# Kernel optimization log

Measured on AMD Instinct MI355X. Metric: run time of the kernel, lower is better.

Reference implementation:

```python
import jax, jax.numpy as jnp
import numpy as np

B, L1, D, H = 4, 1024, 512, 16
L, R = 8192, 8
DFF = 4 * D
DH = D // H  # head dim = 32


def _ln(x, g, b, eps=1e-5):
    mu = x.mean(-1, keepdims=True)
    var = ((x - mu) ** 2).mean(-1, keepdims=True)
    return (x - mu) * jax.lax.rsqrt(var + eps) * g + b


def _mha(q_in, k_in, v_in, Wq, bq, Wk, bk, Wv, bv, Wo, bo):
    # Informer FullAttention (mask_flag=False), scale = 1/sqrt(head_dim), mix=False
    Bq, Lq, _ = q_in.shape
    S = k_in.shape[1]
    q = (q_in @ Wq.T + bq).reshape(Bq, Lq, H, DH)
    k = (k_in @ Wk.T + bk).reshape(Bq, S, H, DH)
    v = (v_in @ Wv.T + bv).reshape(Bq, S, H, DH)
    scores = jnp.einsum('blhe,bshe->bhls', q, k) * (1.0 / jnp.sqrt(jnp.float32(DH)))
    A = jax.nn.softmax(scores, axis=-1)
    out = jnp.einsum('bhls,bshd->blhd', A, v).reshape(Bq, Lq, D)
    return out @ Wo.T + bo


def _p(key, *shape):
    return jax.random.normal(key, shape, jnp.float32) * 0.02


def setup_inputs() -> dict:
    ks = jax.random.split(jax.random.key(0), 16)
    inp = {
        'x': jax.random.normal(ks[0], (B, L1, D), jnp.float32),
        'global_feat': jax.random.normal(ks[1], (B, D, L), jnp.float32),
        'conv_w': _p(ks[2], D, D), 'conv_b': jnp.zeros((D,), jnp.float32),
        'sWq': _p(ks[3], D, D), 'sbq': jnp.zeros((D,), jnp.float32),
        'sWk': _p(ks[4], D, D), 'sbk': jnp.zeros((D,), jnp.float32),
        'sWv': _p(ks[5], D, D), 'sbv': jnp.zeros((D,), jnp.float32),
        'sWo': _p(ks[6], D, D), 'sbo': jnp.zeros((D,), jnp.float32),
        'cWq': _p(ks[7], D, D), 'cbq': jnp.zeros((D,), jnp.float32),
        'cWk': _p(ks[8], D, D), 'cbk': jnp.zeros((D,), jnp.float32),
        'cWv': _p(ks[9], D, D), 'cbv': jnp.zeros((D,), jnp.float32),
        'cWo': _p(ks[10], D, D), 'cbo': jnp.zeros((D,), jnp.float32),
        'ffn_w1': _p(ks[11], DFF, D), 'ffn_b1': jnp.zeros((DFF,), jnp.float32),
        'ffn_w2': _p(ks[12], D, DFF), 'ffn_b2': jnp.zeros((D,), jnp.float32),
        'ln1_g': jnp.ones((D,), jnp.float32), 'ln1_b': jnp.zeros((D,), jnp.float32),
        'ln2_g': jnp.ones((D,), jnp.float32), 'ln2_b': jnp.zeros((D,), jnp.float32),
        'ln3_g': jnp.ones((D,), jnp.float32), 'ln3_b': jnp.zeros((D,), jnp.float32),
    }
    return inp


def reference(x, global_feat, conv_w, conv_b,
              sWq, sbq, sWk, sbk, sWv, sbv, sWo, sbo,
              cWq, cbq, cWk, cbk, cWv, cbv, cWo, cbo,
              ffn_w1, ffn_b1, ffn_w2, ffn_b2,
              ln1_g, ln1_b, ln2_g, ln2_b, ln3_g, ln3_b):
    b, c, length = global_feat.shape
    win = 2 * R  # step == window_size -> non-overlapping windows
    nw = (length - win) // win + 1
    w = global_feat[:, :, :nw * win].reshape(b, c, nw, win)
    # norm over singleton last dim == |max - min| per (b, c, window)
    stat = jnp.abs(w.max(-1) - w.min(-1))  # [B, C, NW]
    # pointwise Conv1d(512,512,1) + relu
    res = jax.nn.relu(jnp.einsum('oc,bcn->bon', conv_w, stat) + conv_b[None, :, None])
    cross = res.transpose(0, 2, 1)  # [B, NW, D] tokens for cross attention
    # EncoderLayer3: self-attn -> cross-attn -> FFN, post-LN residuals
    h = _ln(x + _mha(x, x, x, sWq, sbq, sWk, sbk, sWv, sbv, sWo, sbo), ln1_g, ln1_b)
    h = _ln(h + _mha(h, cross, cross, cWq, cbq, cWk, cbk, cWv, cbv, cWo, cbo), ln2_g, ln2_b)
    y = jax.nn.gelu(h @ ffn_w1.T + ffn_b1) @ ffn_w2.T + ffn_b2
    out = _ln(h + y, ln3_g, ln3_b)
    return out.transpose(0, 2, 1)  # [B, D, L1]
```

## Files before the change

kernel.cpp:

```cpp
#include <hip/hip_runtime.h>
#include <stdint.h>
#include <math.h>


typedef short  s16x8 __attribute__((ext_vector_type(8)));
typedef float  f32x4 __attribute__((ext_vector_type(4)));

__device__ inline unsigned short f2bf(float f) {
  uint32_t u = __builtin_bit_cast(uint32_t, f);
  u += 0x7fffu + ((u >> 16) & 1u);
  return (unsigned short)(u >> 16);
}
__device__ inline float bf2f(unsigned short h) {
  uint32_t u = ((uint32_t)h) << 16;
  return __builtin_bit_cast(float, u);
}
__device__ inline uint32_t cvtpk_bf16(float lo, float hi) {
  uint32_t r;
  asm("v_cvt_pk_bf16_f32 %0, %1, %2" : "=v"(r) : "v"(lo), "v"(hi));
  return r;
}

#define QSCALE 0.25503486611627154f

__global__ __launch_bounds__(256) void convert_bf16_kernel(
    const float* s0, const float* s1, const float* s2, const float* s3,
    const float* s4, const float* s5, const float* s6, const float* s7,
    const float* s8, const float* s9, const float* s10, const float* s11,
    unsigned short* dst) {
  const size_t cum[13] = {0, 262144, 524288, 786432, 1048576, 1310720,
                          1572864, 1835008, 2097152, 2359296, 3407872,
                          4456448, 6553600};
  const float* srcs[12] = {s0, s1, s2, s3, s4, s5, s6, s7, s8, s9, s10, s11};
  size_t e0 = ((size_t)blockIdx.x * 256 + threadIdx.x) * 8;
  int seg = 0;
  while (e0 >= cum[seg + 1]) ++seg;
  const float* sp = srcs[seg] + (e0 - cum[seg]);
  float4 a = *(const float4*)sp;
  float4 b = *(const float4*)(sp + 4);
  unsigned short o[8] = {f2bf(a.x), f2bf(a.y), f2bf(a.z), f2bf(a.w),
                         f2bf(b.x), f2bf(b.y), f2bf(b.z), f2bf(b.w)};
  *(uint4*)&dst[e0] = *(const uint4*)o;
}

__global__ __launch_bounds__(256) void window_stat_kernel(
    const float* __restrict__ gf, unsigned short* __restrict__ statT) {
  int gidx = blockIdx.x * 256 + threadIdx.x;
  int c = gidx & 511;
  int n = (gidx >> 9) & 511;
  int b = gidx >> 18;
  const float4* p = (const float4*)(gf + ((size_t)(b * 512 + c) << 13) + n * 16);
  float4 w0 = p[0], w1 = p[1], w2 = p[2], w3 = p[3];
  float mx = w0.x, mn = w0.x;
  float vals[15] = {w0.y, w0.z, w0.w, w1.x, w1.y, w1.z, w1.w,
                    w2.x, w2.y, w2.z, w2.w, w3.x, w3.y, w3.z, w3.w};
#pragma unroll
  for (int i = 0; i < 15; ++i) {
    mx = fmaxf(mx, vals[i]);
    mn = fminf(mn, vals[i]);
  }
  statT[((size_t)(b * 512 + n) << 9) + c] = f2bf(mx - mn);
}

__global__ __launch_bounds__(256) void biascat_kernel(
    const float* __restrict__ sbq, const float* __restrict__ sbk,
    const float* __restrict__ sbv, const float* __restrict__ cbk,
    const float* __restrict__ cbv, float* __restrict__ dst) {
  int i = blockIdx.x * 256 + threadIdx.x;
  float v;
  if (i < 512) v = sbq[i];
  else if (i < 1024) v = sbk[i - 512];
  else if (i < 1536) v = sbv[i - 1024];
  else if (i < 2048) v = cbk[i - 1536];
  else v = cbv[i - 2048];
  dst[i] = v;
}

template <int ACT, int OUTBF, int SCALEQ>
__global__ __launch_bounds__(256) void gemm_bf16(
    const unsigned short* __restrict__ A, const unsigned short* __restrict__ W,
    const float* __restrict__ bias, void* __restrict__ Cout,
    int M, int N, int K) {
  __shared__ __align__(16) unsigned short As[2][64 * 32];
  __shared__ __align__(16) unsigned short Bs[2][128 * 32];
  const int t = threadIdx.x;
  const int w = t >> 6, lane = t & 63;
  const int r = lane & 15, g = lane >> 4;
  const int wm = w >> 1, wn = w & 1;
  const int m0 = blockIdx.y * 64, n0 = blockIdx.x * 128;

  auto STAGE = [&](int buf, int k0) {
    {
      int row = t >> 2, seg = t & 3;
      const unsigned short* ga = A + (size_t)(m0 + row) * K + k0 + seg * 8;
      __builtin_amdgcn_global_load_lds(
          (const __attribute__((address_space(1))) uint32_t*)ga,
          (__attribute__((address_space(3))) uint32_t*)&As[buf][t * 8], 16, 0, 0);
    }
#pragma unroll
    for (int ii = 0; ii < 2; ++ii) {
      int c = t + 256 * ii;
      int row = c >> 2, seg = c & 3;
      const unsigned short* gb = W + (size_t)(n0 + row) * K + k0 + seg * 8;
      __builtin_amdgcn_global_load_lds(
          (const __attribute__((address_space(1))) uint32_t*)gb,
          (__attribute__((address_space(3))) uint32_t*)&Bs[buf][c * 8], 16, 0, 0);
    }
  };

  f32x4 acc[2][4];
#pragma unroll
  for (int mi = 0; mi < 2; ++mi)
#pragma unroll
    for (int ni = 0; ni < 4; ++ni) acc[mi][ni] = (f32x4){0.f, 0.f, 0.f, 0.f};

  STAGE(0, 0);
  __syncthreads();
  int cur = 0;
  for (int k0 = 0; k0 < K; k0 += 32) {
    if (k0 + 32 < K) STAGE(cur ^ 1, k0 + 32);
    s16x8 af[2], bf[4];
#pragma unroll
    for (int mi = 0; mi < 2; ++mi)
      af[mi] = *(const s16x8*)&As[cur][(wm * 32 + mi * 16 + r) * 32 + g * 8];
#pragma unroll
    for (int ni = 0; ni < 4; ++ni)
      bf[ni] = *(const s16x8*)&Bs[cur][(wn * 64 + ni * 16 + r) * 32 + g * 8];
#pragma unroll
    for (int mi = 0; mi < 2; ++mi)
#pragma unroll
      for (int ni = 0; ni < 4; ++ni)
        acc[mi][ni] = __builtin_amdgcn_mfma_f32_16x16x32_bf16(
            af[mi], bf[ni], acc[mi][ni], 0, 0, 0);
    __syncthreads();
    cur ^= 1;
  }

#pragma unroll
  for (int ni = 0; ni < 4; ++ni) {
    const int col = n0 + wn * 64 + ni * 16 + r;
    const float bv = bias[col];
#pragma unroll
    for (int mi = 0; mi < 2; ++mi) {
#pragma unroll
      for (int rg = 0; rg < 4; ++rg) {
        const int row = m0 + wm * 32 + mi * 16 + g * 4 + rg;
        float v = acc[mi][ni][rg] + bv;
        if (ACT == 1) v = fmaxf(v, 0.f);
        if (ACT == 2) {
          float u = 0.7978845608028654f * (v + 0.044715f * v * v * v);
          float e = __expf(2.f * u);
          float th = 1.f - 2.f / (e + 1.f);
          v = 0.5f * v * (1.f + th);
        }
        if (SCALEQ && col < 512) v *= QSCALE;
        if (OUTBF)
          ((unsigned short*)Cout)[(size_t)row * N + col] = f2bf(v);
        else
          ((float*)Cout)[(size_t)row * N + col] = v;
      }
    }
  }
}

template <int S>
__global__ __launch_bounds__(256) void vtrans_kernel(
    const unsigned short* __restrict__ V, int vstride,
    unsigned short* __restrict__ VT) {
  const int b = blockIdx.z, h = blockIdx.y, s0 = blockIdx.x * 64;
  const int t = threadIdx.x;
  __shared__ unsigned short tile[64 * 40];
  {
    int i = t >> 2, seg = t & 3;
    *(uint4*)&tile[i * 40 + seg * 8] =
        *(const uint4*)&V[((size_t)(b * S + s0 + i)) * vstride + h * 32 + seg * 8];
  }
  __syncthreads();
  {
    int d = t >> 3, j = t & 7;
    unsigned short vals[8];
#pragma unroll
    for (int u = 0; u < 8; ++u) vals[u] = tile[(j * 8 + u) * 40 + d];
    *(uint4*)&VT[((size_t)((b * 16 + h) * 32 + d)) * S + s0 + j * 8] =
        *(const uint4*)vals;
  }
}

template <int S>
__global__ __launch_bounds__(512) void attn_mfma(
    const unsigned short* __restrict__ Q, int qstride,
    const unsigned short* __restrict__ K, int kstride,
    const unsigned short* __restrict__ VT, unsigned short* __restrict__ O) {
  constexpr int NT = S / 128;
  __shared__ __align__(16) unsigned short Kl[128 * 40];
  __shared__ __align__(16) unsigned short Vl[32 * 136];
  __shared__ __align__(16) unsigned short Pl[8][16 * 136];
  const int t = threadIdx.x;
  const int w = t >> 6, lane = t & 63;
  const int r = lane & 15, g = lane >> 4;
  const int qt = blockIdx.x, h = blockIdx.y, b = blockIdx.z;
  const int q0 = qt * 128 + w * 16;

  s16x8 qa = *(const s16x8*)&Q[((size_t)(b * 1024 + q0 + r)) * qstride + h * 32 + g * 8];

  f32x4 o0 = (f32x4){0.f, 0.f, 0.f, 0.f};
  f32x4 o1 = (f32x4){0.f, 0.f, 0.f, 0.f};
  float m = -1e30f, l = 0.f;

  for (int nt = 0; nt < NT; ++nt) {
    const int kv0 = nt * 128;
    {
      int row = t >> 2, seg = t & 3;
      *(uint4*)&Kl[row * 40 + seg * 8] =
          *(const uint4*)&K[((size_t)(b * S + kv0 + row)) * kstride + h * 32 + seg * 8];
    }
    {
      int d = t >> 4, sc = t & 15;
      *(uint4*)&Vl[d * 136 + sc * 8] =
          *(const uint4*)&VT[((size_t)((b * 16 + h) * 32 + d)) * S + kv0 + sc * 8];
    }
    __syncthreads();

    f32x4 s[8];
#pragma unroll
    for (int nb = 0; nb < 8; ++nb) {
      s16x8 ka = *(const s16x8*)&Kl[(nb * 16 + r) * 40 + g * 8];
      s[nb] = __builtin_amdgcn_mfma_f32_16x16x32_bf16(
          ka, qa, (f32x4){0.f, 0.f, 0.f, 0.f}, 0, 0, 0);
    }

    float tm = -1e30f;
#pragma unroll
    for (int nb = 0; nb < 8; ++nb) {
      float a01 = fmaxf(s[nb][0], s[nb][1]);
      float a23 = fmaxf(s[nb][2], s[nb][3]);
      tm = fmaxf(tm, fmaxf(a01, a23));
    }
    tm = fmaxf(tm, __shfl_xor(tm, 16));
    tm = fmaxf(tm, __shfl_xor(tm, 32));
    const float mnew = fmaxf(m, tm);
    const float corr = __builtin_amdgcn_exp2f(m - mnew);
    float ps = 0.f;
#pragma unroll
    for (int nb = 0; nb < 8; ++nb) {
      float p0 = __builtin_amdgcn_exp2f(s[nb][0] - mnew);
      float p1 = __builtin_amdgcn_exp2f(s[nb][1] - mnew);
      float p2 = __builtin_amdgcn_exp2f(s[nb][2] - mnew);
      float p3 = __builtin_amdgcn_exp2f(s[nb][3] - mnew);
      ps += (p0 + p1) + (p2 + p3);
      uint2 pv;
      pv.x = cvtpk_bf16(p0, p1);
      pv.y = cvtpk_bf16(p2, p3);
      *(uint2*)&Pl[w][r * 136 + nb * 16 + g * 4] = pv;
    }
    ps += __shfl_xor(ps, 16);
    ps += __shfl_xor(ps, 32);
    l = l * corr + ps;
    m = mnew;
#pragma unroll
    for (int rg = 0; rg < 4; ++rg) { o0[rg] *= corr; o1[rg] *= corr; }

#pragma unroll
    for (int ks = 0; ks < 4; ++ks) {
      s16x8 va0 = *(const s16x8*)&Vl[r * 136 + ks * 32 + g * 8];
      s16x8 va1 = *(const s16x8*)&Vl[(16 + r) * 136 + ks * 32 + g * 8];
      s16x8 pb  = *(const s16x8*)&Pl[w][r * 136 + ks * 32 + g * 8];
      o0 = __builtin_amdgcn_mfma_f32_16x16x32_bf16(va0, pb, o0, 0, 0, 0);
      o1 = __builtin_amdgcn_mfma_f32_16x16x32_bf16(va1, pb, o1, 0, 0, 0);
    }
    __syncthreads();
  }

  const float inv = 1.f / l;
  const size_t row = (size_t)(b * 1024 + q0 + r);
  uint2 w0, w1;
  w0.x = cvtpk_bf16(o0[0] * inv, o0[1] * inv);
  w0.y = cvtpk_bf16(o0[2] * inv, o0[3] * inv);
  w1.x = cvtpk_bf16(o1[0] * inv, o1[1] * inv);
  w1.y = cvtpk_bf16(o1[2] * inv, o1[3] * inv);
  *(uint2*)&O[row * 512 + h * 32 + g * 4]      = w0;
  *(uint2*)&O[row * 512 + h * 32 + 16 + g * 4] = w1;
}

template <int XBF, int ABF, int MODE>
__global__ __launch_bounds__(256) void ln_kernel(
    const void* __restrict__ X, const void* __restrict__ A,
    const float* __restrict__ gw, const float* __restrict__ bw,
    void* __restrict__ O) {
  const int rr = blockIdx.x;
  const int t = threadIdx.x;
  const size_t base = (size_t)rr * 512;
  float x0, x1, a0, a1;
  if (XBF) {
    x0 = bf2f(((const unsigned short*)X)[base + t]);
    x1 = bf2f(((const unsigned short*)X)[base + t + 256]);
  } else {
    x0 = ((const float*)X)[base + t];
    x1 = ((const float*)X)[base + t + 256];
  }
  if (ABF) {
    a0 = bf2f(((const unsigned short*)A)[base + t]);
    a1 = bf2f(((const unsigned short*)A)[base + t + 256]);
  } else {
    a0 = ((const float*)A)[base + t];
    a1 = ((const float*)A)[base + t + 256];
  }
  float v0 = x0 + a0;
  float v1 = x1 + a1;
  __shared__ float wsum[4];
  float s = v0 + v1;
#pragma unroll
  for (int of = 32; of; of >>= 1) s += __shfl_down(s, of);
  if ((t & 63) == 0) wsum[t >> 6] = s;
  __syncthreads();
  const float mean = (wsum[0] + wsum[1] + wsum[2] + wsum[3]) * (1.f / 512.f);
  __syncthreads();
  float d0 = v0 - mean, d1 = v1 - mean;
  float s2 = d0 * d0 + d1 * d1;
#pragma unroll
  for (int of = 32; of; of >>= 1) s2 += __shfl_down(s2, of);
  if ((t & 63) == 0) wsum[t >> 6] = s2;
  __syncthreads();
  const float var = (wsum[0] + wsum[1] + wsum[2] + wsum[3]) * (1.f / 512.f);
  const float rstd = rsqrtf(var + 1e-5f);
  float o0 = d0 * rstd * gw[t] + bw[t];
  float o1 = d1 * rstd * gw[t + 256] + bw[t + 256];
  if (MODE == 0) {
    ((unsigned short*)O)[base + t] = f2bf(o0);
    ((unsigned short*)O)[base + t + 256] = f2bf(o1);
  } else {
    int b = rr >> 10, l = rr & 1023;
    ((float*)O)[((size_t)(b * 512) + t) * 1024 + l] = o0;
    ((float*)O)[((size_t)(b * 512) + t + 256) * 1024 + l] = o1;
  }
}

extern "C" void kernel_launch(void* const* d_in, const int* in_sizes, int n_in,
                              void* d_out, int out_size, void* d_ws, size_t ws_size,
                              hipStream_t stream) {
  const float* x      = (const float*)d_in[0];
  const float* gf     = (const float*)d_in[1];
  const float* conv_w = (const float*)d_in[2];
  const float* conv_b = (const float*)d_in[3];
  const float* sWq = (const float*)d_in[4],  *sbq = (const float*)d_in[5];
  const float* sWk = (const float*)d_in[6],  *sbk = (const float*)d_in[7];
  const float* sWv = (const float*)d_in[8],  *sbv = (const float*)d_in[9];
  const float* sWo = (const float*)d_in[10], *sbo = (const float*)d_in[11];
  const float* cWq = (const float*)d_in[12], *cbq = (const float*)d_in[13];
  const float* cWk = (const float*)d_in[14], *cbk = (const float*)d_in[15];
  const float* cWv = (const float*)d_in[16], *cbv = (const float*)d_in[17];
  const float* cWo = (const float*)d_in[18], *cbo = (const float*)d_in[19];
  const float* fw1 = (const float*)d_in[20], *fb1 = (const float*)d_in[21];
  const float* fw2 = (const float*)d_in[22], *fb2 = (const float*)d_in[23];
  const float* ln1_g = (const float*)d_in[24], *ln1_b = (const float*)d_in[25];
  const float* ln2_g = (const float*)d_in[26], *ln2_b = (const float*)d_in[27];
  const float* ln3_g = (const float*)d_in[28], *ln3_b = (const float*)d_in[29];
  float* out = (float*)d_out;

  unsigned short* bfp = (unsigned short*)d_ws;
  unsigned short* conv_wb = bfp + 0;
  unsigned short* sWqb = bfp + 262144;
  unsigned short* cWqb = bfp + 1310720;
  unsigned short* cWkb = bfp + 1572864;
  unsigned short* cWob = bfp + 2097152;
  unsigned short* sWob = bfp + 1048576;
  unsigned short* fw1b = bfp + 2359296, *fw2b = bfp + 3407872;
  unsigned short* xbf  = bfp + 4456448;

  unsigned short* SC   = bfp + 6553600;
  unsigned short* qkvb = SC;
  unsigned short* ckvb = SC + 6291456;
  unsigned short* qcb  = SC + 8388608;
  unsigned short* vtb  = SC + 10485760;
  unsigned short* ctxb = SC + 12582912;
  unsigned short* projb= SC + 14680064;
  unsigned short* hbf  = SC + 16777216;
  unsigned short* h2bf = SC + 18874368;
  unsigned short* statTb = qcb;
  unsigned short* crossb = ctxb;
  unsigned short* midb   = qkvb;
  float* biasf = (float*)projb;

  convert_bf16_kernel<<<3200, 256, 0, stream>>>(
      conv_w, sWq, sWk, sWv, sWo, cWq, cWk, cWv, cWo, fw1, fw2, x, bfp);
  window_stat_kernel<<<4096, 256, 0, stream>>>(gf, statTb);
  biascat_kernel<<<10, 256, 0, stream>>>(sbq, sbk, sbv, cbk, cbv, biasf);

  gemm_bf16<1, 1, 0><<<dim3(4, 32), 256, 0, stream>>>(
      statTb, conv_wb, conv_b, crossb, 2048, 512, 512);
  gemm_bf16<0, 1, 1><<<dim3(12, 64), 256, 0, stream>>>(
      xbf, sWqb, biasf, qkvb, 4096, 1536, 512);
  gemm_bf16<0, 1, 0><<<dim3(8, 32), 256, 0, stream>>>(
      crossb, cWkb, biasf + 1536, ckvb, 2048, 1024, 512);

  vtrans_kernel<1024><<<dim3(16, 16, 4), 256, 0, stream>>>(qkvb + 1024, 1536, vtb);
  attn_mfma<1024><<<dim3(8, 16, 4), 512, 0, stream>>>(
      qkvb, 1536, qkvb + 512, 1536, vtb, ctxb);
  gemm_bf16<0, 1, 0><<<dim3(4, 64), 256, 0, stream>>>(
      ctxb, sWob, sbo, projb, 4096, 512, 512);
  ln_kernel<0, 1, 0><<<4096, 256, 0, stream>>>(x, projb, ln1_g, ln1_b, hbf);

  gemm_bf16<0, 1, 1><<<dim3(4, 64), 256, 0, stream>>>(
      hbf, cWqb, cbq, qcb, 4096, 512, 512);
  vtrans_kernel<512><<<dim3(8, 16, 4), 256, 0, stream>>>(ckvb + 512, 1024, vtb);
  attn_mfma<512><<<dim3(8, 16, 4), 512, 0, stream>>>(
      qcb, 512, ckvb, 1024, vtb, ctxb);
  gemm_bf16<0, 1, 0><<<dim3(4, 64), 256, 0, stream>>>(
      ctxb, cWob, cbo, projb, 4096, 512, 512);
  ln_kernel<1, 1, 0><<<4096, 256, 0, stream>>>(hbf, projb, ln2_g, ln2_b, h2bf);

  gemm_bf16<2, 1, 0><<<dim3(16, 64), 256, 0, stream>>>(
      h2bf, fw1b, fb1, midb, 4096, 2048, 512);
  gemm_bf16<0, 1, 0><<<dim3(4, 64), 256, 0, stream>>>(
      midb, fw2b, fb2, projb, 4096, 512, 2048);
  ln_kernel<1, 1, 1><<<4096, 256, 0, stream>>>(h2bf, projb, ln3_g, ln3_b, out);
}
```

Measured before the change: 380.3 us.

## Merge prep kernels, widen GEMM K-tile with swizzle, fuse V transpose, tile output transpose

Folds the bf16 conversion, window-stat and bias-concat launches into one prep kernel. The GEMM K-step grows from 32 to 64, with an XOR-swizzled LDS layout to avoid bank conflicts. Attention now reads V directly, transposes it into LDS and prefetches the next K/V tile into registers, which drops the separate vtrans launches. The final LayerNorm writes bf16 and a tiled transpose kernel produces the fp32 output, replacing the strided scattered stores. In exchange, LDS use per GEMM block doubles and the output is rounded to bf16 before the transpose, which costs some precision.

```diff
diff --git a/kernel.cpp b/kernel.cpp
--- a/kernel.cpp
+++ b/kernel.cpp
@@ -23,57 +23,58 @@
 
 #define QSCALE 0.25503486611627154f
 
-__global__ __launch_bounds__(256) void convert_bf16_kernel(
+__global__ __launch_bounds__(256) void prep_kernel(
     const float* s0, const float* s1, const float* s2, const float* s3,
     const float* s4, const float* s5, const float* s6, const float* s7,
     const float* s8, const float* s9, const float* s10, const float* s11,
-    unsigned short* dst) {
-  const size_t cum[13] = {0, 262144, 524288, 786432, 1048576, 1310720,
-                          1572864, 1835008, 2097152, 2359296, 3407872,
-                          4456448, 6553600};
-  const float* srcs[12] = {s0, s1, s2, s3, s4, s5, s6, s7, s8, s9, s10, s11};
-  size_t e0 = ((size_t)blockIdx.x * 256 + threadIdx.x) * 8;
-  int seg = 0;
-  while (e0 >= cum[seg + 1]) ++seg;
-  const float* sp = srcs[seg] + (e0 - cum[seg]);
-  float4 a = *(const float4*)sp;
-  float4 b = *(const float4*)(sp + 4);
-  unsigned short o[8] = {f2bf(a.x), f2bf(a.y), f2bf(a.z), f2bf(a.w),
-                         f2bf(b.x), f2bf(b.y), f2bf(b.z), f2bf(b.w)};
-  *(uint4*)&dst[e0] = *(const uint4*)o;
-}
-
-__global__ __launch_bounds__(256) void window_stat_kernel(
-    const float* __restrict__ gf, unsigned short* __restrict__ statT) {
-  int gidx = blockIdx.x * 256 + threadIdx.x;
-  int c = gidx & 511;
-  int n = (gidx >> 9) & 511;
-  int b = gidx >> 18;
-  const float4* p = (const float4*)(gf + ((size_t)(b * 512 + c) << 13) + n * 16);
-  float4 w0 = p[0], w1 = p[1], w2 = p[2], w3 = p[3];
-  float mx = w0.x, mn = w0.x;
-  float vals[15] = {w0.y, w0.z, w0.w, w1.x, w1.y, w1.z, w1.w,
-                    w2.x, w2.y, w2.z, w2.w, w3.x, w3.y, w3.z, w3.w};
-#pragma unroll
-  for (int i = 0; i < 15; ++i) {
-    mx = fmaxf(mx, vals[i]);
-    mn = fminf(mn, vals[i]);
-  }
-  statT[((size_t)(b * 512 + n) << 9) + c] = f2bf(mx - mn);
-}
-
-__global__ __launch_bounds__(256) void biascat_kernel(
+    unsigned short* dst,
+    const float* __restrict__ gf, unsigned short* __restrict__ statT,
     const float* __restrict__ sbq, const float* __restrict__ sbk,
     const float* __restrict__ sbv, const float* __restrict__ cbk,
-    const float* __restrict__ cbv, float* __restrict__ dst) {
-  int i = blockIdx.x * 256 + threadIdx.x;
-  float v;
-  if (i < 512) v = sbq[i];
-  else if (i < 1024) v = sbk[i - 512];
-  else if (i < 1536) v = sbv[i - 1024];
-  else if (i < 2048) v = cbk[i - 1536];
-  else v = cbv[i - 2048];
-  dst[i] = v;
+    const float* __restrict__ cbv, float* __restrict__ biasf) {
+  const int bid = blockIdx.x;
+  const int t = threadIdx.x;
+  if (bid < 3200) {
+    const size_t cum[13] = {0, 262144, 524288, 786432, 1048576, 1310720,
+                            1572864, 1835008, 2097152, 2359296, 3407872,
+                            4456448, 6553600};
+    const float* srcs[12] = {s0, s1, s2, s3, s4, s5, s6, s7, s8, s9, s10, s11};
+    size_t e0 = ((size_t)bid * 256 + t) * 8;
+    int seg = 0;
+    while (e0 >= cum[seg + 1]) ++seg;
+    const float* sp = srcs[seg] + (e0 - cum[seg]);
+    float4 a = *(const float4*)sp;
+    float4 b = *(const float4*)(sp + 4);
+    unsigned short o[8] = {f2bf(a.x), f2bf(a.y), f2bf(a.z), f2bf(a.w),
+                           f2bf(b.x), f2bf(b.y), f2bf(b.z), f2bf(b.w)};
+    *(uint4*)&dst[e0] = *(const uint4*)o;
+  } else if (bid < 7296) {
+    int gidx = (bid - 3200) * 256 + t;
+    int c = gidx & 511;
+    int n = (gidx >> 9) & 511;
+    int b = gidx >> 18;
+    const float4* p = (const float4*)(gf + ((size_t)(b * 512 + c) << 13) + n * 16);
+    float4 w0 = p[0], w1 = p[1], w2 = p[2], w3 = p[3];
+    float mx = w0.x, mn = w0.x;
+    float vals[15] = {w0.y, w0.z, w0.w, w1.x, w1.y, w1.z, w1.w,
+                      w2.x, w2.y, w2.z, w2.w, w3.x, w3.y, w3.z, w3.w};
+#pragma unroll
+    for (int i = 0; i < 15; ++i) {
+      mx = fmaxf(mx, vals[i]);
+      mn = fminf(mn, vals[i]);
+    }
+    statT[((size_t)(b * 512 + n) << 9) + c] = f2bf(mx - mn);
+  } else {
+    for (int i = t; i < 2560; i += 256) {
+      float v;
+      if (i < 512) v = sbq[i];
+      else if (i < 1024) v = sbk[i - 512];
+      else if (i < 1536) v = sbv[i - 1024];
+      else if (i < 2048) v = cbk[i - 1536];
+      else v = cbv[i - 2048];
+      biasf[i] = v;
+    }
+  }
 }
 
 template <int ACT, int OUTBF, int SCALEQ>
@@ -81,8 +82,8 @@
     const unsigned short* __restrict__ A, const unsigned short* __restrict__ W,
     const float* __restrict__ bias, void* __restrict__ Cout,
     int M, int N, int K) {
-  __shared__ __align__(16) unsigned short As[2][64 * 32];
-  __shared__ __align__(16) unsigned short Bs[2][128 * 32];
+  __shared__ __align__(16) unsigned short As[2][64 * 64];
+  __shared__ __align__(16) unsigned short Bs[2][128 * 64];
   const int t = threadIdx.x;
   const int w = t >> 6, lane = t & 63;
   const int r = lane & 15, g = lane >> 4;
@@ -90,18 +91,22 @@
   const int m0 = blockIdx.y * 64, n0 = blockIdx.x * 128;
 
   auto STAGE = [&](int buf, int k0) {
-    {
-      int row = t >> 2, seg = t & 3;
-      const unsigned short* ga = A + (size_t)(m0 + row) * K + k0 + seg * 8;
+#pragma unroll
+    for (int ii = 0; ii < 2; ++ii) {
+      int c = t + 256 * ii;
+      int row = c >> 3, sc = c & 7;
+      const unsigned short* ga =
+          A + (size_t)(m0 + row) * K + k0 + ((sc ^ (row & 7)) << 3);
       __builtin_amdgcn_global_load_lds(
           (const __attribute__((address_space(1))) uint32_t*)ga,
-          (__attribute__((address_space(3))) uint32_t*)&As[buf][t * 8], 16, 0, 0);
-    }
-#pragma unroll
-    for (int ii = 0; ii < 2; ++ii) {
+          (__attribute__((address_space(3))) uint32_t*)&As[buf][c * 8], 16, 0, 0);
+    }
+#pragma unroll
+    for (int ii = 0; ii < 4; ++ii) {
       int c = t + 256 * ii;
-      int row = c >> 2, seg = c & 3;
-      const unsigned short* gb = W + (size_t)(n0 + row) * K + k0 + seg * 8;
+      int row = c >> 3, sc = c & 7;
+      const unsigned short* gb =
+          W + (size_t)(n0 + row) * K + k0 + ((sc ^ (row & 7)) << 3);
       __builtin_amdgcn_global_load_lds(
           (const __attribute__((address_space(1))) uint32_t*)gb,
           (__attribute__((address_space(3))) uint32_t*)&Bs[buf][c * 8], 16, 0, 0);
@@ -117,21 +122,26 @@
   STAGE(0, 0);
   __syncthreads();
   int cur = 0;
-  for (int k0 = 0; k0 < K; k0 += 32) {
-    if (k0 + 32 < K) STAGE(cur ^ 1, k0 + 32);
-    s16x8 af[2], bf[4];
-#pragma unroll
-    for (int mi = 0; mi < 2; ++mi)
-      af[mi] = *(const s16x8*)&As[cur][(wm * 32 + mi * 16 + r) * 32 + g * 8];
-#pragma unroll
-    for (int ni = 0; ni < 4; ++ni)
-      bf[ni] = *(const s16x8*)&Bs[cur][(wn * 64 + ni * 16 + r) * 32 + g * 8];
-#pragma unroll
-    for (int mi = 0; mi < 2; ++mi)
+  for (int k0 = 0; k0 < K; k0 += 64) {
+    if (k0 + 64 < K) STAGE(cur ^ 1, k0 + 64);
+#pragma unroll
+    for (int ks = 0; ks < 2; ++ks) {
+      s16x8 af[2], bf[4];
+#pragma unroll
+      for (int mi = 0; mi < 2; ++mi)
+        af[mi] = *(const s16x8*)&As[cur][(wm * 32 + mi * 16 + r) * 64 +
+                                         (((ks * 4 + g) ^ (r & 7)) << 3)];
 #pragma unroll
       for (int ni = 0; ni < 4; ++ni)
-        acc[mi][ni] = __builtin_amdgcn_mfma_f32_16x16x32_bf16(
-            af[mi], bf[ni], acc[mi][ni], 0, 0, 0);
+        bf[ni] = *(const s16x8*)&Bs[cur][(wn * 64 + ni * 16 + r) * 64 +
+                                         (((ks * 4 + g) ^ (r & 7)) << 3)];
+#pragma unroll
+      for (int mi = 0; mi < 2; ++mi)
+#pragma unroll
+        for (int ni = 0; ni < 4; ++ni)
+          acc[mi][ni] = __builtin_amdgcn_mfma_f32_16x16x32_bf16(
+              af[mi], bf[ni], acc[mi][ni], 0, 0, 0);
+    }
     __syncthreads();
     cur ^= 1;
   }
@@ -164,33 +174,11 @@
 }
 
 template <int S>
-__global__ __launch_bounds__(256) void vtrans_kernel(
-    const unsigned short* __restrict__ V, int vstride,
-    unsigned short* __restrict__ VT) {
-  const int b = blockIdx.z, h = blockIdx.y, s0 = blockIdx.x * 64;
-  const int t = threadIdx.x;
-  __shared__ unsigned short tile[64 * 40];
-  {
-    int i = t >> 2, seg = t & 3;
-    *(uint4*)&tile[i * 40 + seg * 8] =
-        *(const uint4*)&V[((size_t)(b * S + s0 + i)) * vstride + h * 32 + seg * 8];
-  }
-  __syncthreads();
-  {
-    int d = t >> 3, j = t & 7;
-    unsigned short vals[8];
-#pragma unroll
-    for (int u = 0; u < 8; ++u) vals[u] = tile[(j * 8 + u) * 40 + d];
-    *(uint4*)&VT[((size_t)((b * 16 + h) * 32 + d)) * S + s0 + j * 8] =
-        *(const uint4*)vals;
-  }
-}
-
-template <int S>
 __global__ __launch_bounds__(512) void attn_mfma(
     const unsigned short* __restrict__ Q, int qstride,
     const unsigned short* __restrict__ K, int kstride,
-    const unsigned short* __restrict__ VT, unsigned short* __restrict__ O) {
+    const unsigned short* __restrict__ V, int vstride,
+    unsigned short* __restrict__ O) {
   constexpr int NT = S / 128;
   __shared__ __align__(16) unsigned short Kl[128 * 40];
   __shared__ __align__(16) unsigned short Vl[32 * 136];
@@ -200,6 +188,7 @@
   const int r = lane & 15, g = lane >> 4;
   const int qt = blockIdx.x, h = blockIdx.y, b = blockIdx.z;
   const int q0 = qt * 128 + w * 16;
+  const int kvr = t >> 2, dsg = t & 3;
 
   s16x8 qa = *(const s16x8*)&Q[((size_t)(b * 1024 + q0 + r)) * qstride + h * 32 + g * 8];
 
@@ -207,18 +196,24 @@
   f32x4 o1 = (f32x4){0.f, 0.f, 0.f, 0.f};
   float m = -1e30f, l = 0.f;
 
+  uint4 kA = {}, vA = {}, kB = {}, vB = {};
+  auto GLOAD = [&](int nt, uint4& kr, uint4& vr) {
+    const int kv0 = nt * 128;
+    kr = *(const uint4*)&K[((size_t)(b * S + kv0 + kvr)) * kstride + h * 32 + dsg * 8];
+    vr = *(const uint4*)&V[((size_t)(b * S + kv0 + kvr)) * vstride + h * 32 + dsg * 8];
+  };
+  GLOAD(0, kA, vA);
+
   for (int nt = 0; nt < NT; ++nt) {
-    const int kv0 = nt * 128;
+    __syncthreads();
+    *(uint4*)&Kl[kvr * 40 + dsg * 8] = kA;
     {
-      int row = t >> 2, seg = t & 3;
-      *(uint4*)&Kl[row * 40 + seg * 8] =
-          *(const uint4*)&K[((size_t)(b * S + kv0 + row)) * kstride + h * 32 + seg * 8];
-    }
-    {
-      int d = t >> 4, sc = t & 15;
-      *(uint4*)&Vl[d * 136 + sc * 8] =
-          *(const uint4*)&VT[((size_t)((b * 16 + h) * 32 + d)) * S + kv0 + sc * 8];
-    }
+      unsigned short vs[8];
+      *(uint4*)vs = vA;
+#pragma unroll
+      for (int u = 0; u < 8; ++u) Vl[(dsg * 8 + u) * 136 + kvr] = vs[u];
+    }
+    if (nt + 1 < NT) GLOAD(nt + 1, kB, vB);
     __syncthreads();
 
     f32x4 s[8];
@@ -268,7 +263,7 @@
       o0 = __builtin_amdgcn_mfma_f32_16x16x32_bf16(va0, pb, o0, 0, 0, 0);
       o1 = __builtin_amdgcn_mfma_f32_16x16x32_bf16(va1, pb, o1, 0, 0, 0);
     }
-    __syncthreads();
+    kA = kB; vA = vB;
   }
 
   const float inv = 1.f / l;
@@ -282,11 +277,11 @@
   *(uint2*)&O[row * 512 + h * 32 + 16 + g * 4] = w1;
 }
 
-template <int XBF, int ABF, int MODE>
+template <int XBF, int ABF>
 __global__ __launch_bounds__(256) void ln_kernel(
     const void* __restrict__ X, const void* __restrict__ A,
     const float* __restrict__ gw, const float* __restrict__ bw,
-    void* __restrict__ O) {
+    unsigned short* __restrict__ O) {
   const int rr = blockIdx.x;
   const int t = threadIdx.x;
   const size_t base = (size_t)rr * 512;
@@ -323,15 +318,33 @@
   __syncthreads();
   const float var = (wsum[0] + wsum[1] + wsum[2] + wsum[3]) * (1.f / 512.f);
   const float rstd = rsqrtf(var + 1e-5f);
-  float o0 = d0 * rstd * gw[t] + bw[t];
-  float o1 = d1 * rstd * gw[t + 256] + bw[t + 256];
-  if (MODE == 0) {
-    ((unsigned short*)O)[base + t] = f2bf(o0);
-    ((unsigned short*)O)[base + t + 256] = f2bf(o1);
-  } else {
-    int b = rr >> 10, l = rr & 1023;
-    ((float*)O)[((size_t)(b * 512) + t) * 1024 + l] = o0;
-    ((float*)O)[((size_t)(b * 512) + t + 256) * 1024 + l] = o1;
+  O[base + t] = f2bf(d0 * rstd * gw[t] + bw[t]);
+  O[base + t + 256] = f2bf(d1 * rstd * gw[t + 256] + bw[t + 256]);
+}
+
+__global__ __launch_bounds__(256) void transpose_out_kernel(
+    const unsigned short* __restrict__ h3, float* __restrict__ out) {
+  __shared__ float tile[64][65];
+  const int t = threadIdx.x;
+  const int lt = blockIdx.x * 64, ct = blockIdx.y * 64, b = blockIdx.z;
+#pragma unroll
+  for (int ii = 0; ii < 2; ++ii) {
+    int idx = t + 256 * ii;
+    int row = idx >> 3, ch = idx & 7;
+    uint4 v = *(const uint4*)&h3[((size_t)(b * 1024 + lt + row)) * 512 + ct + ch * 8];
+    unsigned short vs[8];
+    *(uint4*)vs = v;
+#pragma unroll
+    for (int u = 0; u < 8; ++u) tile[row][ch * 8 + u] = bf2f(vs[u]);
+  }
+  __syncthreads();
+  const int c = t >> 2, l0 = (t & 3) * 16;
+  float* op = &out[((size_t)(b * 512 + ct + c)) * 1024 + lt + l0];
+#pragma unroll
+  for (int i = 0; i < 4; ++i) {
+    float4 o4 = {tile[l0 + i * 4 + 0][c], tile[l0 + i * 4 + 1][c],
+                 tile[l0 + i * 4 + 2][c], tile[l0 + i * 4 + 3][c]};
+    *(float4*)(op + i * 4) = o4;
   }
 }
 
@@ -371,7 +384,6 @@
   unsigned short* qkvb = SC;
   unsigned short* ckvb = SC + 6291456;
   unsigned short* qcb  = SC + 8388608;
-  unsigned short* vtb  = SC + 10485760;
   unsigned short* ctxb = SC + 12582912;
   unsigned short* projb= SC + 14680064;
   unsigned short* hbf  = SC + 16777216;
@@ -381,10 +393,9 @@
   unsigned short* midb   = qkvb;
   float* biasf = (float*)projb;
 
-  convert_bf16_kernel<<<3200, 256, 0, stream>>>(
-      conv_w, sWq, sWk, sWv, sWo, cWq, cWk, cWv, cWo, fw1, fw2, x, bfp);
-  window_stat_kernel<<<4096, 256, 0, stream>>>(gf, statTb);
-  biascat_kernel<<<10, 256, 0, stream>>>(sbq, sbk, sbv, cbk, cbv, biasf);
+  prep_kernel<<<7297, 256, 0, stream>>>(
+      conv_w, sWq, sWk, sWv, sWo, cWq, cWk, cWv, cWo, fw1, fw2, x, bfp,
+      gf, statTb, sbq, sbk, sbv, cbk, cbv, biasf);
 
   gemm_bf16<1, 1, 0><<<dim3(4, 32), 256, 0, stream>>>(
       statTb, conv_wb, conv_b, crossb, 2048, 512, 512);
@@ -393,25 +404,24 @@
   gemm_bf16<0, 1, 0><<<dim3(8, 32), 256, 0, stream>>>(
       crossb, cWkb, biasf + 1536, ckvb, 2048, 1024, 512);
 
-  vtrans_kernel<1024><<<dim3(16, 16, 4), 256, 0, stream>>>(qkvb + 1024, 1536, vtb);
   attn_mfma<1024><<<dim3(8, 16, 4), 512, 0, stream>>>(
-      qkvb, 1536, qkvb + 512, 1536, vtb, ctxb);
+      qkvb, 1536, qkvb + 512, 1536, qkvb + 1024, 1536, ctxb);
   gemm_bf16<0, 1, 0><<<dim3(4, 64), 256, 0, stream>>>(
       ctxb, sWob, sbo, projb, 4096, 512, 512);
-  ln_kernel<0, 1, 0><<<4096, 256, 0, stream>>>(x, projb, ln1_g, ln1_b, hbf);
+  ln_kernel<0, 1><<<4096, 256, 0, stream>>>(x, projb, ln1_g, ln1_b, hbf);
 
   gemm_bf16<0, 1, 1><<<dim3(4, 64), 256, 0, stream>>>(
       hbf, cWqb, cbq, qcb, 4096, 512, 512);
-  vtrans_kernel<512><<<dim3(8, 16, 4), 256, 0, stream>>>(ckvb + 512, 1024, vtb);
   attn_mfma<512><<<dim3(8, 16, 4), 512, 0, stream>>>(
-      qcb, 512, ckvb, 1024, vtb, ctxb);
+      qcb, 512, ckvb, 1024, ckvb + 512, 1024, ctxb);
   gemm_bf16<0, 1, 0><<<dim3(4, 64), 256, 0, stream>>>(
       ctxb, cWob, cbo, projb, 4096, 512, 512);
-  ln_kernel<1, 1, 0><<<4096, 256, 0, stream>>>(hbf, projb, ln2_g, ln2_b, h2bf);
+  ln_kernel<1, 1><<<4096, 256, 0, stream>>>(hbf, projb, ln2_g, ln2_b, h2bf);
 
   gemm_bf16<2, 1, 0><<<dim3(16, 64), 256, 0, stream>>>(
       h2bf, fw1b, fb1, midb, 4096, 2048, 512);
   gemm_bf16<0, 1, 0><<<dim3(4, 64), 256, 0, stream>>>(
       midb, fw2b, fb2, projb, 4096, 512, 2048);
-  ln_kernel<1, 1, 1><<<4096, 256, 0, stream>>>(h2bf, projb, ln3_g, ln3_b, out);
-}
+  ln_kernel<1, 1><<<4096, 256, 0, stream>>>(h2bf, projb, ln3_g, ln3_b, hbf);
+  transpose_out_kernel<<<dim3(16, 8, 4), 256, 0, stream>>>(hbf, out);
+}
```

After: 351.9 us. -7.5%, faster.
